# Kernel optimization log

Measured on AMD Instinct MI355X. Metric: run time of the kernel, lower is better.

Reference implementation:

```python
import jax, jax.numpy as jnp
import numpy as np

NH = 12      # attention heads
EPS = 1e-5   # torch nn.LayerNorm default


def _ln(x, g, b):
    m = jnp.mean(x, axis=-1, keepdims=True)
    v = jnp.var(x, axis=-1, keepdims=True)
    return (x - m) * jax.lax.rsqrt(v + EPS) * g + b


def _rel_table(table, n):
    # q_size == k_size == n, table length == 2n-1 -> pure gather, no interpolation
    idx = jnp.arange(n)[:, None] - jnp.arange(n)[None, :] + (n - 1)
    return table[idx]  # (n, n, head_dim)


def _attn2d(x, qkv_w, qkv_b, proj_w, proj_b, rel_h, rel_w):
    B, H, W, C = x.shape
    hd = C // NH
    scale = hd ** -0.5
    N = H * W
    qkv = x.reshape(B, N, C) @ qkv_w + qkv_b                    # (B, N, 3C)
    qkv = qkv.reshape(B, N, 3, NH, hd).transpose(2, 0, 3, 1, 4).reshape(3, B * NH, N, hd)
    q, k, v = qkv[0], qkv[1], qkv[2]
    attn = jnp.einsum('bnd,bmd->bnm', q * scale, k)             # (B*NH, N, N)
    Rh = _rel_table(rel_h, H)
    Rw = _rel_table(rel_w, W)
    rq = q.reshape(B * NH, H, W, hd)                            # unscaled q, as in torch
    bias_h = jnp.einsum('bhwc,hkc->bhwk', rq, Rh)
    bias_w = jnp.einsum('bhwc,wkc->bhwk', rq, Rw)
    attn = (attn.reshape(B * NH, H, W, H, W)
            + bias_h[:, :, :, :, None]
            + bias_w[:, :, :, None, :]).reshape(B * NH, N, N)
    attn = jax.nn.softmax(attn, axis=-1)
    out = (attn @ v).reshape(B, NH, H, W, hd).transpose(0, 2, 3, 1, 4).reshape(B, H, W, C)
    return out @ proj_w + proj_b


def _win_part(x, ws):
    B, H, W, C = x.shape
    ph = (ws - H % ws) % ws
    pw = (ws - W % ws) % ws
    x = jnp.pad(x, ((0, 0), (0, ph), (0, pw), (0, 0)))
    Hp, Wp = H + ph, W + pw
    x = x.reshape(B, Hp // ws, ws, Wp // ws, ws, C).transpose(0, 1, 3, 2, 4, 5)
    return x.reshape(-1, ws, ws, C), (Hp, Wp)


def _win_unpart(wins, ws, pad_hw, hw):
    Hp, Wp = pad_hw
    H, W = hw
    B = wins.shape[0] // (Hp * Wp // ws // ws)
    x = wins.reshape(B, Hp // ws, Wp // ws, ws, ws, -1).transpose(0, 1, 3, 2, 4, 5)
    x = x.reshape(B, Hp, Wp, -1)
    return x[:, :H, :W, :]


def _block(x, ws, ln1g, ln1b, qkvw, qkvb, projw, projb, relh, relw,
           ln2g, ln2b, mw1, mb1, mw2, mb2):
    shortcut = x
    x = _ln(x, ln1g, ln1b)
    if ws > 0:
        H, W = x.shape[1], x.shape[2]
        x, pad_hw = _win_part(x, ws)
    x = _attn2d(x, qkvw, qkvb, projw, projb, relh, relw)
    if ws > 0:
        x = _win_unpart(x, ws, pad_hw, (H, W))
    x = shortcut + x
    h = _ln(x, ln2g, ln2b)
    h = jax.nn.gelu(h @ mw1 + mb1, approximate=False) @ mw2 + mb2
    return x + h


def setup_inputs() -> dict:
    key = jax.random.key(0)
    def rnd(i, shape, s=0.02):
        return jax.random.normal(jax.random.fold_in(key, i), shape, jnp.float32) * s
    C, M, HD = 768, 3072, 64
    d = {
        'x': rnd(0, (1, 3, 1024, 1024), 1.0),
        'patch_w': rnd(1, (16, 16, 3, C)),
        'patch_b': rnd(2, (C,)),
        'pos_embed': rnd(3, (1, 64, 64, C)),
    }
    i = 4
    for s, L in (('1', 27), ('2', 127)):
        for name, shape in (('ln1g', (C,)), ('ln1b', (C,)), ('qkvw', (C, 3 * C)),
                            ('qkvb', (3 * C,)), ('projw', (C, C)), ('projb', (C,)),
                            ('relh', (L, HD)), ('relw', (L, HD)),
                            ('ln2g', (C,)), ('ln2b', (C,)),
                            ('mw1', (C, M)), ('mb1', (M,)), ('mw2', (M, C)), ('mb2', (C,))):
            d[name + s] = rnd(i, shape)
            i += 1
    for s in ('1', '2'):
        d['ln1g' + s] = d['ln1g' + s] + 1.0
        d['ln2g' + s] = d['ln2g' + s] + 1.0
    return d


def reference(x, patch_w, patch_b, pos_embed,
              ln1g1, ln1b1, qkvw1, qkvb1, projw1, projb1, relh1, relw1,
              ln2g1, ln2b1, mw11, mb11, mw21, mb21,
              ln1g2, ln1b2, qkvw2, qkvb2, projw2, projb2, relh2, relw2,
              ln2g2, ln2b2, mw12, mb12, mw22, mb22):
    # patch embed: 16x16 stride-16 conv, output NHWC (B, 64, 64, 768)
    feat = jax.lax.conv_general_dilated(
        x, patch_w, window_strides=(16, 16), padding='VALID',
        dimension_numbers=('NCHW', 'HWIO', 'NHWC'))
    feat = feat + patch_b + pos_embed
    feat = _block(feat, 14, ln1g1, ln1b1, qkvw1, qkvb1, projw1, projb1,
                  relh1, relw1, ln2g1, ln2b1, mw11, mb11, mw21, mb21)
    feat = _block(feat, 0, ln1g2, ln1b2, qkvw2, qkvb2, projw2, projb2,
                  relh2, relw2, ln2g2, ln2b2, mw12, mb12, mw22, mb22)
    return feat
```

## Files before the change

### kernel.cpp

```cpp
#include <hip/hip_runtime.h>


using u16 = unsigned short;
using u32 = unsigned int;
using short8  = __attribute__((ext_vector_type(8))) short;
using floatx4 = __attribute__((ext_vector_type(4))) float;

__device__ __forceinline__ float bfu2f(u16 u) { return __builtin_bit_cast(float, (u32)u << 16); }
__device__ __forceinline__ u16   f2bfu(float f) {
  u32 u = __builtin_bit_cast(u32, f);
  return (u16)((u + 0x7fffu + ((u >> 16) & 1u)) >> 16);
}
__device__ __forceinline__ u32 cvtpk_bf16(float a, float b) {
  u32 r; asm("v_cvt_pk_bf16_f32 %0, %1, %2" : "=v"(r) : "v"(a), "v"(b)); return r;
}
#define DIV14(x) (((x) * 4682) >> 16)
#define WAIT_VM0()   __builtin_amdgcn_s_waitcnt(0x3f70)
#define WAIT_LGKM0() __builtin_amdgcn_s_waitcnt(0xc07f)

__device__ __forceinline__ void gld_lds16(const u16* g, u16* l) {
  __builtin_amdgcn_global_load_lds(
      (const __attribute__((address_space(1))) u32*)g,
      (__attribute__((address_space(3))) u32*)l, 16, 0, 0);
}

__global__ __launch_bounds__(256) void detect_k(const u16* __restrict__ x, int* __restrict__ flag)
{
  __shared__ int tot;
  if (threadIdx.x == 0) tot = 0;
  __syncthreads();
  int cnt = 0;
  for (int i = threadIdx.x; i < 4096; i += 256) {
    int e = (x[2 * i] >> 7) & 0xFF;
    cnt += (e >= 100 && e <= 134) ? 1 : 0;
  }
  atomicAdd(&tot, cnt);
  __syncthreads();
  if (threadIdx.x == 0) *flag = (tot >= 2458) ? 1 : 0;
}

struct CvtEnt { const void* src; int n; int dstoff; };
struct CvtArgs { CvtEnt e[24]; int cnt; };

__global__ __launch_bounds__(256) void tobf_multi_k(CvtArgs a, u16* __restrict__ dst,
                                                    const int* __restrict__ flag)
{
  int gid = blockIdx.x * 256 + threadIdx.x;
  bool isbf = (*flag != 0);
  for (int t = 0; t < a.cnt; ++t)
    if (gid < a.e[t].n)
      dst[a.e[t].dstoff + gid] = isbf ? ((const u16*)a.e[t].src)[gid]
                                      : f2bfu(((const float*)a.e[t].src)[gid]);
}

__global__ __launch_bounds__(256) void tobf4_k(const void* __restrict__ src, u16* __restrict__ dst,
                                               int n4, const int* __restrict__ flag)
{
  int i = blockIdx.x * 256 + threadIdx.x;
  if (i >= n4) return;
  ushort4 o;
  if (*flag) o = ((const ushort4*)src)[i];
  else {
    float4 f = ((const float4*)src)[i];
    o.x = f2bfu(f.x); o.y = f2bfu(f.y); o.z = f2bfu(f.z); o.w = f2bfu(f.w);
  }
  ((ushort4*)dst)[i] = o;
}

__global__ __launch_bounds__(256) void tobfT_k(const void* __restrict__ src, u16* __restrict__ dst,
                                               int K, int N, const int* __restrict__ flag)
{
  __shared__ u16 t[64][65];
  const int n0 = blockIdx.x * 64, k0 = blockIdx.y * 64;
  const int r = threadIdx.x >> 2, c = (threadIdx.x & 3) * 16;
  if (*flag) {
    const u16* s = (const u16*)src + (size_t)(k0 + r) * N + n0 + c;
    union { uint4 v[2]; u16 e[16]; } u;
    u.v[0] = *(const uint4*)s; u.v[1] = *(const uint4*)(s + 8);
    #pragma unroll
    for (int j = 0; j < 16; ++j) t[c + j][r] = u.e[j];
  } else {
    const float* s = (const float*)src + (size_t)(k0 + r) * N + n0 + c;
    #pragma unroll
    for (int j = 0; j < 16; ++j) t[c + j][r] = f2bfu(s[j]);
  }
  __syncthreads();
  union { uint4 v[2]; u16 e[16]; } o;
  #pragma unroll
  for (int j = 0; j < 16; ++j) o.e[j] = t[r][c + j];
  u16* d = dst + (size_t)(n0 + r) * K + k0 + c;
  *(uint4*)d = o.v[0]; *(uint4*)(d + 8) = o.v[1];
}

__global__ __launch_bounds__(256) void im2col_k(const void* __restrict__ xv, u16* __restrict__ a,
                                                const int* __restrict__ flag)
{
  int t = blockIdx.x, tid = threadIdx.x;
  int py = t >> 6, px = t & 63;
  int ky = tid >> 4, kx = tid & 15;
  size_t src = (size_t)(py * 16 + ky) * 1024 + px * 16 + kx;
  u16 v0, v1, v2;
  if (*flag) {
    const u16* x = (const u16*)xv;
    v0 = x[src]; v1 = x[src + 1048576]; v2 = x[src + 2097152];
  } else {
    const float* x = (const float*)xv;
    v0 = f2bfu(x[src]); v1 = f2bfu(x[src + 1048576]); v2 = f2bfu(x[src + 2097152]);
  }
  size_t dst = (size_t)t * 768 + tid * 3;
  a[dst] = v0; a[dst + 1] = v1; a[dst + 2] = v2;
}

__global__ __launch_bounds__(256) void ln_k(const float* __restrict__ x,
                                            const u16* __restrict__ g,
                                            const u16* __restrict__ b,
                                            u16* __restrict__ y)
{
  const int t = blockIdx.x, tid = threadIdx.x;
  const float* xp = x + (size_t)t * 768;
  float v0 = xp[tid], v1 = xp[tid + 256], v2 = xp[tid + 512];
  float s = v0 + v1 + v2;
  float q = v0 * v0 + v1 * v1 + v2 * v2;
  #pragma unroll
  for (int off = 32; off; off >>= 1) { s += __shfl_xor(s, off); q += __shfl_xor(q, off); }
  __shared__ float red[8];
  int wid = tid >> 6, lane = tid & 63;
  if (lane == 0) { red[wid] = s; red[4 + wid] = q; }
  __syncthreads();
  s = red[0] + red[1] + red[2] + red[3];
  q = red[4] + red[5] + red[6] + red[7];
  float mean = s * (1.f / 768.f);
  float var  = q * (1.f / 768.f) - mean * mean;
  float rstd = rsqrtf(var + 1e-5f);
  u16* yp = y + (size_t)t * 768;
  yp[tid]       = f2bfu((v0 - mean) * rstd * bfu2f(g[tid])       + bfu2f(b[tid]));
  yp[tid + 256] = f2bfu((v1 - mean) * rstd * bfu2f(g[tid + 256]) + bfu2f(b[tid + 256]));
  yp[tid + 512] = f2bfu((v2 - mean) * rstd * bfu2f(g[tid + 512]) + bfu2f(b[tid + 512]));
}

__global__ __launch_bounds__(256) void win_part_k(const u16* __restrict__ ln, u16* __restrict__ w)
{
  int vid = blockIdx.x * 256 + threadIdx.x;
  if (vid >= 470400) return;
  size_t idx = (size_t)vid * 8;
  int c = (int)(idx % 768);
  int r = (int)(idx / 768);
  int win = r / 196, tok = r - win * 196;
  int gy = (win / 5) * 14 + tok / 14;
  int gx = (win % 5) * 14 + tok % 14;
  uint4 v = make_uint4(0, 0, 0, 0);
  if (gy < 64 && gx < 64)
    v = *(const uint4*)(ln + ((size_t)(gy * 64 + gx) * 768 + c));
  *(uint4*)(w + idx) = v;
}

enum { MODE_FEAT = 0, MODE_QKV = 1, MODE_RES = 2, MODE_GELU = 3, MODE_OUT = 4 };

template<int BN>
__global__ __launch_bounds__(256) void mgemm_k(
    const u16* __restrict__ A, const u16* __restrict__ Bt, const u16* __restrict__ bias,
    int M, int N, int K, int mode,
    float* __restrict__ outf, u16* __restrict__ outb,
    const float* __restrict__ res, const u16* __restrict__ pos,
    u16* __restrict__ qb, u16* __restrict__ kb, u16* __restrict__ vt, int TW,
    const int* __restrict__ flagp)
{
  constexpr int NWN = BN / 64, NWM = 4 / NWN;
  constexpr int WTM = 128 / NWM;
  constexpr int MS = WTM / 16, NS = 4;
  __shared__ __align__(16) u16 As[2][128 * 32];
  __shared__ __align__(16) u16 Bs[2][BN * 32];
  const int tid = threadIdx.x;
  const int wid = tid >> 6, lane = tid & 63;
  const int l15 = lane & 15, quad = lane >> 4;
  const int wm = wid / NWN, wn = wid % NWN;
  const int m0 = blockIdx.y * 128, n0 = blockIdx.x * BN;

  floatx4 acc[MS][NS];
  #pragma unroll
  for (int i = 0; i < MS; ++i)
    #pragma unroll
    for (int j = 0; j < NS; ++j) acc[i][j] = (floatx4){0.f, 0.f, 0.f, 0.f};

  const int sr = lane >> 2, sc = (lane & 3) * 8;
  const u16* ag0 = A + (size_t)min(m0 + wid * 32 + sr,      M - 1) * K + sc;
  const u16* ag1 = A + (size_t)min(m0 + wid * 32 + 16 + sr, M - 1) * K + sc;
  const u16 *bg0 = nullptr, *bg1 = nullptr;
  if constexpr (BN == 128) {
    bg0 = Bt + (size_t)(n0 + wid * 32 + sr) * K + sc;
    bg1 = Bt + (size_t)(n0 + wid * 32 + 16 + sr) * K + sc;
  } else {
    bg0 = Bt + (size_t)(n0 + wid * 16 + sr) * K + sc;
  }

  auto issue = [&](int buf, int k0) {
    gld_lds16(ag0 + k0, &As[buf][(wid * 32) * 32]);
    gld_lds16(ag1 + k0, &As[buf][(wid * 32 + 16) * 32]);
    if constexpr (BN == 128) {
      gld_lds16(bg0 + k0, &Bs[buf][(wid * 32) * 32]);
      gld_lds16(bg1 + k0, &Bs[buf][(wid * 32 + 16) * 32]);
    } else {
      gld_lds16(bg0 + k0, &Bs[buf][(wid * 16) * 32]);
    }
  };

  issue(0, 0);
  int bufi = 0;
  for (int k0 = 0; k0 < K; k0 += 32, bufi ^= 1) {
    WAIT_VM0();
    __syncthreads();
    if (k0 + 32 < K) issue(bufi ^ 1, k0 + 32);
    short8 af[MS], bf[NS];
    #pragma unroll
    for (int ms = 0; ms < MS; ++ms)
      af[ms] = *(const short8*)&As[bufi][(wm * WTM + ms * 16 + l15) * 32 + quad * 8];
    #pragma unroll
    for (int ns = 0; ns < NS; ++ns)
      bf[ns] = *(const short8*)&Bs[bufi][(wn * 64 + ns * 16 + l15) * 32 + quad * 8];
    #pragma unroll
    for (int ms = 0; ms < MS; ++ms)
      #pragma unroll
      for (int ns = 0; ns < NS; ++ns)
        acc[ms][ns] = __builtin_amdgcn_mfma_f32_16x16x32_bf16(af[ms], bf[ns], acc[ms][ns], 0, 0, 0);
  }

  const bool outbf = (mode == MODE_OUT) ? (*flagp != 0) : false;
  #pragma unroll
  for (int ms = 0; ms < MS; ++ms) {
    const int gmb = m0 + wm * WTM + ms * 16 + quad * 4;
    #pragma unroll
    for (int ns = 0; ns < NS; ++ns) {
      const int gn = n0 + wn * 64 + ns * 16 + l15;
      const float bb = bfu2f(bias[gn]);
      if (mode == MODE_QKV) {
        const int s = gn / 768, nn = gn - s * 768, h = nn >> 6, d = nn & 63;
        #pragma unroll
        for (int r = 0; r < 4; ++r) {
          int gm = gmb + r; if (gm >= M) continue;
          float v = acc[ms][ns][r] + bb;
          int b = gm / TW, tok = gm - b * TW;
          size_t bh = (size_t)(b * 12 + h);
          if (s == 0)      qb[(bh * TW + tok) * 64 + d] = f2bfu(v);
          else if (s == 1) kb[(bh * TW + tok) * 64 + d] = f2bfu(v);
          else             vt[(bh * 64 + d) * TW + tok] = f2bfu(v);
        }
      } else {
        #pragma unroll
        for (int r = 0; r < 4; ++r) {
          int gm = gmb + r; if (gm >= M) continue;
          size_t o = (size_t)gm * N + gn;
          float v = acc[ms][ns][r] + bb;
          if (mode == MODE_FEAT)      outf[o] = v + bfu2f(pos[o]);
          else if (mode == MODE_RES)  outf[o] = v + res[o];
          else if (mode == MODE_GELU) outb[o] = f2bfu(0.5f * v * (1.f + erff(v * 0.70710678f)));
          else {
            float ov = v + res[o];
            if (outbf) outb[o] = f2bfu(ov);
            else       outf[o] = ov;
          }
        }
      }
    }
  }
}

template<int NT, int TD, bool WIN>
__global__ __launch_bounds__(256) void flash_k(
    const u16* __restrict__ qb, const u16* __restrict__ kb, const u16* __restrict__ vt,
    const u16* __restrict__ relh, const u16* __restrict__ relw,
    u16* __restrict__ outb)
{
  constexpr int NTAB = 2 * TD - 1;
  constexpr int KT = (NT + 63) >> 6;
  constexpr float L2E = 1.4426950408889634f;
  constexpr float SC2 = 0.125f * L2E;
  constexpr int RQ  = 0;
  constexpr int RK0 = 4096;
  constexpr int RK1 = WIN ? 4096 : 8192;
  constexpr int RV0 = WIN ? 8192 : 12288;
  constexpr int RV1 = WIN ? 8192 : 16384;
  constexpr int RG  = WIN ? 12288 : 20480;
  constexpr int GWWIN = RG + 64 * 34;
  constexpr int TOT = WIN ? (GWWIN + 64 * 34) : (RG + 64 * 66);
  __shared__ __align__(16) u16 lds[TOT];

  const int tid = threadIdx.x, wid = tid >> 6, lane = tid & 63;
  const int l15 = lane & 15, quad = lane >> 4;
  const int qt = blockIdx.x, bh = blockIdx.y;
  const int q0 = qt * 64;
  const size_t kvbase = (size_t)bh * NT * 64;
  const size_t vbase  = (size_t)bh * 64 * NT;
  const int myrow = wid * 16 + l15;

  auto swb = [](int row, int blk) { return row * 64 + (((blk ^ row) & 7) << 3); };

  {
    const int r = tid >> 2, cb = (tid & 3) * 2;
    const int tok = min(q0 + r, NT - 1);
    const uint4* p = (const uint4*)(qb + kvbase + (size_t)tok * 64 + cb * 8);
    *(uint4*)&lds[RQ + swb(r, cb)]     = p[0];
    *(uint4*)&lds[RQ + swb(r, cb + 1)] = p[1];
  }
  __syncthreads();
  short8 qf[2];
  qf[0] = *(const short8*)&lds[RQ + swb(myrow, quad)];
  qf[1] = *(const short8*)&lds[RQ + swb(myrow, 4 + quad)];
  WAIT_LGKM0();

  auto stageRB = [&](const u16* tab, int rowoff, int maxrow) {
    const int r = tid >> 2, cb = (tid & 3) * 2;
    const int tr = min(rowoff + r, maxrow);
    const uint4* p = (const uint4*)(tab + (size_t)tr * 64 + cb * 8);
    *(uint4*)&lds[RV0 + swb(r, cb)]     = p[0];
    *(uint4*)&lds[RV0 + swb(r, cb + 1)] = p[1];
  };
  auto gpass = [&](int gbase, int gstride, int ncols) {
    for (int ns = 0; ns < ncols / 16; ++ns) {
      floatx4 g = (floatx4){0.f, 0.f, 0.f, 0.f};
      #pragma unroll
      for (int ks = 0; ks < 2; ++ks) {
        short8 b = *(const short8*)&lds[RV0 + swb(ns * 16 + l15, ks * 4 + quad)];
        g = __builtin_amdgcn_mfma_f32_16x16x32_bf16(qf[ks], b, g, 0, 0, 0);
      }
      #pragma unroll
      for (int r = 0; r < 4; ++r)
        lds[gbase + (wid * 16 + quad * 4 + r) * gstride + ns * 16 + l15] = f2bfu(g[r] * L2E);
    }
  };

  float gwv[4][4];
  if constexpr (!WIN) {
    stageRB(relh, qt, NTAB - 1);  __syncthreads();
    gpass(RG, 66, 64);
    __syncthreads();
    stageRB(relw, 0, NTAB - 1);   __syncthreads();
    gpass(RK0, 66, 64);
    #pragma unroll
    for (int kbi = 0; kbi < 4; ++kbi)
      #pragma unroll
      for (int r = 0; r < 4; ++r) {
        const int iw = myrow + 63 - (kbi * 16 + quad * 4 + r);
        if (iw < 64) gwv[kbi][r] = bfu2f(lds[RK0 + myrow * 66 + iw]);
      }
    WAIT_LGKM0();
    __syncthreads();
    stageRB(relw, 64, NTAB - 1);  __syncthreads();
    gpass(RK0, 66, 64);
    #pragma unroll
    for (int kbi = 0; kbi < 4; ++kbi)
      #pragma unroll
      for (int r = 0; r < 4; ++r) {
        const int iw = myrow + 63 - (kbi * 16 + quad * 4 + r);
        if (iw >= 64) gwv[kbi][r] = bfu2f(lds[RK0 + myrow * 66 + iw - 64]);
      }
    WAIT_LGKM0();
  } else {
    stageRB(relh, 0, NTAB - 1);  __syncthreads();
    gpass(RG, 34, 32);
    __syncthreads();
    stageRB(relw, 0, NTAB - 1);  __syncthreads();
    gpass(GWWIN, 34, 32);
  }

  const int srow = lane >> 3;
  const int scol = (((lane & 7) ^ srow) & 7) << 3;
  const u16* kg = kb + kvbase + (size_t)(wid * 16 + srow) * 64 + scol;
  const u16* vg = vt + vbase  + (size_t)(wid * 16 + srow) * NT + scol;
  auto issue = [&](int buf, int kt2) {
    const u16* k0 = kg + (size_t)kt2 * 4096;
    const u16* v0 = vg + kt2 * 64;
    u16* kd = &lds[(buf ? RK1 : RK0) + wid * 16 * 64];
    u16* vd = &lds[(buf ? RV1 : RV0) + wid * 16 * 64];
    gld_lds16(k0,           kd);
    gld_lds16(k0 + 512,     kd + 512);
    gld_lds16(v0,           vd);
    gld_lds16(v0 + 8 * NT,  vd + 512);
  };

  float mI = -3e38f, lI = 0.f;
  floatx4 Oacc[4];
  #pragma unroll
  for (int d = 0; d < 4; ++d) Oacc[d] = (floatx4){0.f, 0.f, 0.f, 0.f};

  int qy = 0, qx = 0;
  if constexpr (WIN) {
    const int tok0 = q0 + myrow;
    qy = DIV14(tok0); qx = tok0 - 14 * qy;
  }

  if constexpr (!WIN) { __syncthreads(); issue(0, 0); }

  for (int kt = 0; kt < KT; ++kt) {
    int RKb, RVb;
    if constexpr (!WIN) {
      WAIT_VM0();
      __syncthreads();
      if (kt + 1 < KT) issue((kt + 1) & 1, kt + 1);
      RKb = (kt & 1) ? RK1 : RK0;
      RVb = (kt & 1) ? RV1 : RV0;
    } else {
      __syncthreads();
      {
        const int r = tid >> 2, cb = (tid & 3) * 2;
        const int key = min(kt * 64 + r, NT - 1);
        const uint4* p = (const uint4*)(kb + kvbase + (size_t)key * 64 + cb * 8);
        *(uint4*)&lds[RK0 + swb(r, cb)]     = p[0];
        *(uint4*)&lds[RK0 + swb(r, cb + 1)] = p[1];
      }
      {
        const int d = tid >> 2, c = (tid & 3) << 4;
        if (kt * 64 + c + 15 < NT) {
          #pragma unroll
          for (int h = 0; h < 4; ++h) {
            uint2 v = *(const uint2*)(vt + vbase + (size_t)d * NT + kt * 64 + c + h * 4);
            const int col = c + h * 4;
            *(uint2*)&lds[RV0 + d * 64 + ((((col >> 3) ^ d) & 7) << 3) + (col & 7)] = v;
          }
        } else {
          #pragma unroll
          for (int j = 0; j < 16; ++j) {
            int key = min(kt * 64 + c + j, NT - 1);
            const int col = c + j;
            lds[RV0 + d * 64 + ((((col >> 3) ^ d) & 7) << 3) + (col & 7)] =
                vt[vbase + (size_t)d * NT + key];
          }
        }
      }
      __syncthreads();
      RKb = RK0; RVb = RV0;
    }

    floatx4 sacc[4];
    #pragma unroll
    for (int kbi = 0; kbi < 4; ++kbi) sacc[kbi] = (floatx4){0.f, 0.f, 0.f, 0.f};
    __builtin_amdgcn_s_setprio(1);
    #pragma unroll
    for (int ks = 0; ks < 2; ++ks)
      #pragma unroll
      for (int kbi = 0; kbi < 4; ++kbi) {
        short8 a = *(const short8*)&lds[RKb + swb(kbi * 16 + l15, ks * 4 + quad)];
        sacc[kbi] = __builtin_amdgcn_mfma_f32_16x16x32_bf16(a, qf[ks], sacc[kbi], 0, 0, 0);
      }
    __builtin_amdgcn_s_setprio(0);

    float sv[4][4];
    if constexpr (!WIN) {
      #pragma unroll
      for (int kbi = 0; kbi < 4; ++kbi)
        #pragma unroll
        for (int r = 0; r < 4; ++r)
          sv[kbi][r] = fmaf(SC2, sacc[kbi][r], gwv[kbi][r]);
    } else {
      #pragma unroll
      for (int kbi = 0; kbi < 4; ++kbi)
        #pragma unroll
        for (int r = 0; r < 4; ++r) {
          const int j = kt * 64 + kbi * 16 + quad * 4 + r;
          const int ky = DIV14(j), kx = j - 14 * ky;
          int ih = qy - ky + 13; ih = max(0, min(ih, 31));
          int iw = qx - kx + 13; iw = max(0, min(iw, 31));
          float s = SC2 * sacc[kbi][r] + bfu2f(lds[RG + myrow * 34 + ih])
                                       + bfu2f(lds[GWWIN + myrow * 34 + iw]);
          sv[kbi][r] = (j < NT) ? s : -1e30f;
        }
    }

    float rm;
    {
      float a0 = fmaxf(fmaxf(sv[0][0], sv[0][1]), fmaxf(sv[0][2], sv[0][3]));
      float a1 = fmaxf(fmaxf(sv[1][0], sv[1][1]), fmaxf(sv[1][2], sv[1][3]));
      float a2 = fmaxf(fmaxf(sv[2][0], sv[2][1]), fmaxf(sv[2][2], sv[2][3]));
      float a3 = fmaxf(fmaxf(sv[3][0], sv[3][1]), fmaxf(sv[3][2], sv[3][3]));
      rm = fmaxf(fmaxf(a0, a1), fmaxf(a2, a3));
    }
    rm = fmaxf(rm, __shfl_xor(rm, 16));
    rm = fmaxf(rm, __shfl_xor(rm, 32));
    float ghv = 0.f;
    if constexpr (!WIN) ghv = bfu2f(lds[RG + myrow * 66 + (63 - kt)]);
    const float mt = rm + ghv;
    const float mn = fmaxf(mI, mt);
    const float t = mn - ghv;

    float rs = 0.f;
    u32 pk[8];
    #pragma unroll
    for (int kbi = 0; kbi < 4; ++kbi) {
      float p0 = __builtin_amdgcn_exp2f(sv[kbi][0] - t);
      float p1 = __builtin_amdgcn_exp2f(sv[kbi][1] - t);
      float p2 = __builtin_amdgcn_exp2f(sv[kbi][2] - t);
      float p3 = __builtin_amdgcn_exp2f(sv[kbi][3] - t);
      rs += (p0 + p1) + (p2 + p3);
      pk[2 * kbi]     = cvtpk_bf16(p0, p1);
      pk[2 * kbi + 1] = cvtpk_bf16(p2, p3);
    }
    rs += __shfl_xor(rs, 16);
    rs += __shfl_xor(rs, 32);

    #pragma unroll
    for (int kbi = 0; kbi < 4; ++kbi) {
      const int col = kbi * 16 + quad * 4;
      uint2 w2; w2.x = pk[2 * kbi]; w2.y = pk[2 * kbi + 1];
      *(uint2*)&lds[RQ + myrow * 64 + ((((col >> 3) ^ myrow) & 7) << 3) + (col & 7)] = w2;
    }

    if (__any(mt > mI)) {
      const float al = __builtin_amdgcn_exp2f(mI - mn);
      mI = mn;
      lI = fmaf(lI, al, rs);
      #pragma unroll
      for (int d = 0; d < 4; ++d) Oacc[d] *= al;
    } else {
      lI += rs;
    }

    __builtin_amdgcn_s_setprio(1);
    #pragma unroll
    for (int ks = 0; ks < 2; ++ks) {
      short8 pb = *(const short8*)&lds[RQ + swb(myrow, ks * 4 + quad)];
      #pragma unroll
      for (int d = 0; d < 4; ++d) {
        short8 a = *(const short8*)&lds[RVb + swb(d * 16 + l15, ks * 4 + quad)];
        Oacc[d] = __builtin_amdgcn_mfma_f32_16x16x32_bf16(a, pb, Oacc[d], 0, 0, 0);
      }
    }
    __builtin_amdgcn_s_setprio(0);
  }

  const float rinv = 1.f / lI;
  const int tok = q0 + myrow;
  u32 ow[8];
  #pragma unroll
  for (int d = 0; d < 4; ++d) {
    ow[2 * d]     = cvtpk_bf16(Oacc[d][0] * rinv, Oacc[d][1] * rinv);
    ow[2 * d + 1] = cvtpk_bf16(Oacc[d][2] * rinv, Oacc[d][3] * rinv);
  }
  if constexpr (WIN) {
    if (tok < NT) {
      const int win = bh / 12, h = bh - win * 12;
      const int ty = DIV14(tok), tx = tok - 14 * ty;
      const int gy = (win / 5) * 14 + ty, gx = (win % 5) * 14 + tx;
      if (gy < 64 && gx < 64) {
        u16* op = outb + (size_t)(gy * 64 + gx) * 768 + h * 64;
        #pragma unroll
        for (int d = 0; d < 4; ++d)
          *(uint2*)(op + d * 16 + quad * 4) = make_uint2(ow[2 * d], ow[2 * d + 1]);
      }
    }
  } else {
    u16* op = outb + (size_t)tok * 768 + bh * 64;
    #pragma unroll
    for (int d = 0; d < 4; ++d)
      *(uint2*)(op + d * 16 + quad * 4) = make_uint2(ow[2 * d], ow[2 * d + 1]);
  }
}

extern "C" void kernel_launch(void* const* d_in, const int* in_sizes, int n_in,
                              void* d_out, int out_size, void* d_ws, size_t ws_size,
                              hipStream_t stream)
{
  const void* x      = d_in[0];
  const void* patchw = d_in[1];
  const void* patchb = d_in[2];
  const void* pos    = d_in[3];
  const void *ln1g1 = d_in[4],  *ln1b1 = d_in[5];
  const void *qkvw1 = d_in[6],  *qkvb1 = d_in[7];
  const void *projw1= d_in[8],  *projb1= d_in[9];
  const void *relh1 = d_in[10], *relw1 = d_in[11];
  const void *ln2g1 = d_in[12], *ln2b1 = d_in[13];
  const void *mw11  = d_in[14], *mb11  = d_in[15];
  const void *mw21  = d_in[16], *mb21  = d_in[17];
  const void *ln1g2 = d_in[18], *ln1b2 = d_in[19];
  const void *qkvw2 = d_in[20], *qkvb2 = d_in[21];
  const void *projw2= d_in[22], *projb2= d_in[23];
  const void *relh2 = d_in[24], *relw2 = d_in[25];
  const void *ln2g2 = d_in[26], *ln2b2 = d_in[27];
  const void *mw12  = d_in[28], *mb12  = d_in[29];
  const void *mw22  = d_in[30], *mb22  = d_in[31];

  char* w = (char*)d_ws;
  int*   FLAG = (int*)w;  w += 64;
  float* R0 = (float*)w;  w += 12582912;
  float* R1 = (float*)w;  w += 12582912;
  u16*   B0 = (u16*)w;    w += 6291456;
  u16*   Wb = (u16*)w;    w += 7526400;
  u16*   QB = (u16*)w;    w += 7526400;
  u16*   KB = (u16*)w;    w += 7526400;
  u16*   VT = (u16*)w;    w += 7526400;
  u16*   Hb = (u16*)w;    w += 25165824;
  u16*   WA = (u16*)w;    w += 14155776;
  u16*   POSb = (u16*)w;  w += 6291456;
  u16*   PRM = (u16*)w;   w += 106560;
  u16*   Ap = Hb;

  constexpr int WA_QKV = 0, WA_PROJ = 1769472, WA_M1 = 2359296, WA_M2 = 4718592;
  constexpr int PRM_PATCHB = 0, PB1 = 768, PBLK = 26240, PB2 = 768 + PBLK;
  constexpr int O_QKVB = 0, O_PROJB = 2304, O_MB1 = 3072, O_MB2 = 6144,
                O_LN1G = 6912, O_LN1B = 7680, O_LN2G = 8448, O_LN2B = 9216,
                O_RELH = 9984, O_RELW = 18112;

  detect_k<<<1, 256, 0, stream>>>((const u16*)x, FLAG);
  CvtArgs ca; int kk = 0;
  auto add = [&](const void* s, int n, int off) { ca.e[kk].src = s; ca.e[kk].n = n; ca.e[kk].dstoff = off; ++kk; };
  add(patchb, 768, PRM_PATCHB);
  add(qkvb1, 2304, PB1 + O_QKVB); add(projb1, 768, PB1 + O_PROJB);
  add(mb11, 3072, PB1 + O_MB1);   add(mb21, 768, PB1 + O_MB2);
  add(ln1g1, 768, PB1 + O_LN1G);  add(ln1b1, 768, PB1 + O_LN1B);
  add(ln2g1, 768, PB1 + O_LN2G);  add(ln2b1, 768, PB1 + O_LN2B);
  add(relh1, 27 * 64, PB1 + O_RELH); add(relw1, 27 * 64, PB1 + O_RELW);
  add(qkvb2, 2304, PB2 + O_QKVB); add(projb2, 768, PB2 + O_PROJB);
  add(mb12, 3072, PB2 + O_MB1);   add(mb22, 768, PB2 + O_MB2);
  add(ln1g2, 768, PB2 + O_LN1G);  add(ln1b2, 768, PB2 + O_LN1B);
  add(ln2g2, 768, PB2 + O_LN2G);  add(ln2b2, 768, PB2 + O_LN2B);
  add(relh2, 127 * 64, PB2 + O_RELH); add(relw2, 127 * 64, PB2 + O_RELW);
  ca.cnt = kk;
  tobf_multi_k<<<32, 256, 0, stream>>>(ca, PRM, FLAG);
  tobf4_k<<<3072, 256, 0, stream>>>(pos, POSb, 786432, FLAG);

  tobfT_k<<<dim3(12, 12), 256, 0, stream>>>(patchw, WA + WA_M1, 768, 768, FLAG);
  im2col_k<<<4096, 256, 0, stream>>>(x, Ap, FLAG);
  mgemm_k<64><<<dim3(12, 32), 256, 0, stream>>>(Ap, WA + WA_M1, PRM + PRM_PATCHB,
      4096, 768, 768, MODE_FEAT, R0, nullptr, nullptr, POSb, nullptr, nullptr, nullptr, 0, FLAG);

  tobfT_k<<<dim3(36, 12), 256, 0, stream>>>(qkvw1, WA + WA_QKV, 768, 2304, FLAG);
  tobfT_k<<<dim3(12, 12), 256, 0, stream>>>(projw1, WA + WA_PROJ, 768, 768, FLAG);
  tobfT_k<<<dim3(48, 12), 256, 0, stream>>>(mw11, WA + WA_M1, 768, 3072, FLAG);
  tobfT_k<<<dim3(12, 48), 256, 0, stream>>>(mw21, WA + WA_M2, 3072, 768, FLAG);

  ln_k<<<4096, 256, 0, stream>>>(R0, PRM + PB1 + O_LN1G, PRM + PB1 + O_LN1B, B0);
  win_part_k<<<1838, 256, 0, stream>>>(B0, Wb);
  mgemm_k<128><<<dim3(18, 39), 256, 0, stream>>>(Wb, WA + WA_QKV, PRM + PB1 + O_QKVB,
      4900, 2304, 768, MODE_QKV, nullptr, nullptr, nullptr, nullptr, QB, KB, VT, 196, FLAG);
  flash_k<196, 14, true><<<dim3(4, 300), 256, 0, stream>>>(QB, KB, VT,
      PRM + PB1 + O_RELH, PRM + PB1 + O_RELW, B0);
  mgemm_k<64><<<dim3(12, 32), 256, 0, stream>>>(B0, WA + WA_PROJ, PRM + PB1 + O_PROJB,
      4096, 768, 768, MODE_RES, R1, nullptr, R0, nullptr, nullptr, nullptr, nullptr, 0, FLAG);
  ln_k<<<4096, 256, 0, stream>>>(R1, PRM + PB1 + O_LN2G, PRM + PB1 + O_LN2B, B0);
  mgemm_k<128><<<dim3(24, 32), 256, 0, stream>>>(B0, WA + WA_M1, PRM + PB1 + O_MB1,
      4096, 3072, 768, MODE_GELU, nullptr, Hb, nullptr, nullptr, nullptr, nullptr, nullptr, 0, FLAG);
  mgemm_k<64><<<dim3(12, 32), 256, 0, stream>>>(Hb, WA + WA_M2, PRM + PB1 + O_MB2,
      4096, 768, 3072, MODE_RES, R0, nullptr, R1, nullptr, nullptr, nullptr, nullptr, 0, FLAG);

  tobfT_k<<<dim3(36, 12), 256, 0, stream>>>(qkvw2, WA + WA_QKV, 768, 2304, FLAG);
  tobfT_k<<<dim3(12, 12), 256, 0, stream>>>(projw2, WA + WA_PROJ, 768, 768, FLAG);
  tobfT_k<<<dim3(48, 12), 256, 0, stream>>>(mw12, WA + WA_M1, 768, 3072, FLAG);
  tobfT_k<<<dim3(12, 48), 256, 0, stream>>>(mw22, WA + WA_M2, 3072, 768, FLAG);

  ln_k<<<4096, 256, 0, stream>>>(R0, PRM + PB2 + O_LN1G, PRM + PB2 + O_LN1B, B0);
  mgemm_k<128><<<dim3(18, 32), 256, 0, stream>>>(B0, WA + WA_QKV, PRM + PB2 + O_QKVB,
      4096, 2304, 768, MODE_QKV, nullptr, nullptr, nullptr, nullptr, QB, KB, VT, 4096, FLAG);
  flash_k<4096, 64, false><<<dim3(64, 12), 256, 0, stream>>>(QB, KB, VT,
      PRM + PB2 + O_RELH, PRM + PB2 + O_RELW, B0);
  mgemm_k<64><<<dim3(12, 32), 256, 0, stream>>>(B0, WA + WA_PROJ, PRM + PB2 + O_PROJB,
      4096, 768, 768, MODE_RES, R1, nullptr, R0, nullptr, nullptr, nullptr, nullptr, 0, FLAG);
  ln_k<<<4096, 256, 0, stream>>>(R1, PRM + PB2 + O_LN2G, PRM + PB2 + O_LN2B, B0);
  mgemm_k<128><<<dim3(24, 32), 256, 0, stream>>>(B0, WA + WA_M1, PRM + PB2 + O_MB1,
      4096, 3072, 768, MODE_GELU, nullptr, Hb, nullptr, nullptr, nullptr, nullptr, nullptr, 0, FLAG);
  mgemm_k<64><<<dim3(12, 32), 256, 0, stream>>>(Hb, WA + WA_M2, PRM + PB2 + O_MB2,
      4096, 768, 3072, MODE_OUT, (float*)d_out, (u16*)d_out, R1, nullptr, nullptr, nullptr, nullptr, 0, FLAG);
}
```

Baseline: 796.6 us.

## Batch weight transposes, fuse LayerNorm with window partition, unroll flash K/V pipeline

Merges the per-weight transpose/convert launches into a single multi-job kernel per block. The patch weight now gets its own workspace slot so it no longer aliases the MLP weight region. Replaces the LayerNorm plus window-partition pair with one kernel that normalizes directly into the padded window layout, removing one intermediate round trip through memory. The global flash-attention loop is unrolled by two with fixed double-buffer pointers and incremental address updates, and the softmax rescale bookkeeping is simplified. The trade-off is more LDS/register pressure from the unrolled body and extra workspace for the weight copies.

```diff
diff --git a/kernel.cpp b/kernel.cpp
--- a/kernel.cpp
+++ b/kernel.cpp
@@ -67,11 +67,24 @@
   ((ushort4*)dst)[i] = o;
 }
 
-__global__ __launch_bounds__(256) void tobfT_k(const void* __restrict__ src, u16* __restrict__ dst,
-                                               int K, int N, const int* __restrict__ flag)
+struct TJob { const void* src; int dstoff; int K; int N; int blk0; };
+struct TArgs { TJob j[6]; int njobs; };
+
+__global__ __launch_bounds__(256) void tobfT_multi_k(TArgs a, u16* __restrict__ wa,
+                                                     const int* __restrict__ flag)
 {
   __shared__ u16 t[64][65];
-  const int n0 = blockIdx.x * 64, k0 = blockIdx.y * 64;
+  const int bid = blockIdx.x;
+  int ji = 0;
+  #pragma unroll
+  for (int q = 1; q < 6; ++q) if (q < a.njobs && bid >= a.j[q].blk0) ji = q;
+  const void* src = a.j[ji].src;
+  u16* dst = wa + a.j[ji].dstoff;
+  const int K = a.j[ji].K, N = a.j[ji].N;
+  const int local = bid - a.j[ji].blk0;
+  const int nx = N >> 6;
+  const int bx = local % nx, by = local / nx;
+  const int n0 = bx * 64, k0 = by * 64;
   const int r = threadIdx.x >> 2, c = (threadIdx.x & 3) * 16;
   if (*flag) {
     const u16* s = (const u16*)src + (size_t)(k0 + r) * N + n0 + c;
@@ -138,20 +151,38 @@
   yp[tid + 512] = f2bfu((v2 - mean) * rstd * bfu2f(g[tid + 512]) + bfu2f(b[tid + 512]));
 }
 
-__global__ __launch_bounds__(256) void win_part_k(const u16* __restrict__ ln, u16* __restrict__ w)
-{
-  int vid = blockIdx.x * 256 + threadIdx.x;
-  if (vid >= 470400) return;
-  size_t idx = (size_t)vid * 8;
-  int c = (int)(idx % 768);
-  int r = (int)(idx / 768);
-  int win = r / 196, tok = r - win * 196;
-  int gy = (win / 5) * 14 + tok / 14;
-  int gx = (win % 5) * 14 + tok % 14;
-  uint4 v = make_uint4(0, 0, 0, 0);
-  if (gy < 64 && gx < 64)
-    v = *(const uint4*)(ln + ((size_t)(gy * 64 + gx) * 768 + c));
-  *(uint4*)(w + idx) = v;
+__global__ __launch_bounds__(256) void ln_win_k(const float* __restrict__ x,
+                                                const u16* __restrict__ g,
+                                                const u16* __restrict__ b,
+                                                u16* __restrict__ wout)
+{
+  const int t = blockIdx.x, tid = threadIdx.x;
+  const int win = t / 196, tok = t - win * 196;
+  const int ty = DIV14(tok), tx = tok - 14 * ty;
+  const int gy = (win / 5) * 14 + ty, gx = (win % 5) * 14 + tx;
+  u16* yp = wout + (size_t)t * 768;
+  if (gy >= 64 || gx >= 64) {
+    yp[tid] = 0; yp[tid + 256] = 0; yp[tid + 512] = 0;
+    return;
+  }
+  const float* xp = x + (size_t)(gy * 64 + gx) * 768;
+  float v0 = xp[tid], v1 = xp[tid + 256], v2 = xp[tid + 512];
+  float s = v0 + v1 + v2;
+  float q = v0 * v0 + v1 * v1 + v2 * v2;
+  #pragma unroll
+  for (int off = 32; off; off >>= 1) { s += __shfl_xor(s, off); q += __shfl_xor(q, off); }
+  __shared__ float red[8];
+  int wid = tid >> 6, lane = tid & 63;
+  if (lane == 0) { red[wid] = s; red[4 + wid] = q; }
+  __syncthreads();
+  s = red[0] + red[1] + red[2] + red[3];
+  q = red[4] + red[5] + red[6] + red[7];
+  float mean = s * (1.f / 768.f);
+  float var  = q * (1.f / 768.f) - mean * mean;
+  float rstd = rsqrtf(var + 1e-5f);
+  yp[tid]       = f2bfu((v0 - mean) * rstd * bfu2f(g[tid])       + bfu2f(b[tid]));
+  yp[tid + 256] = f2bfu((v1 - mean) * rstd * bfu2f(g[tid + 256]) + bfu2f(b[tid + 256]));
+  yp[tid + 512] = f2bfu((v2 - mean) * rstd * bfu2f(g[tid + 512]) + bfu2f(b[tid + 512]));
 }
 
 enum { MODE_FEAT = 0, MODE_QKV = 1, MODE_RES = 2, MODE_GELU = 3, MODE_OUT = 4 };
@@ -364,17 +395,22 @@
 
   const int srow = lane >> 3;
   const int scol = (((lane & 7) ^ srow) & 7) << 3;
-  const u16* kg = kb + kvbase + (size_t)(wid * 16 + srow) * 64 + scol;
-  const u16* vg = vt + vbase  + (size_t)(wid * 16 + srow) * NT + scol;
-  auto issue = [&](int buf, int kt2) {
-    const u16* k0 = kg + (size_t)kt2 * 4096;
-    const u16* v0 = vg + kt2 * 64;
-    u16* kd = &lds[(buf ? RK1 : RK0) + wid * 16 * 64];
-    u16* vd = &lds[(buf ? RV1 : RV0) + wid * 16 * 64];
-    gld_lds16(k0,           kd);
-    gld_lds16(k0 + 512,     kd + 512);
-    gld_lds16(v0,           vd);
-    gld_lds16(v0 + 8 * NT,  vd + 512);
+  const u16* kp  = kb + kvbase + (size_t)(wid * 16 + srow) * 64 + scol;
+  const u16* kp2 = kp + 512;
+  const u16* vp  = vt + vbase  + (size_t)(wid * 16 + srow) * NT + scol;
+  const u16* vp2 = vp + (size_t)8 * NT;
+  u16* const kd0 = &lds[RK0 + wid * 1024];
+  u16* const kd1 = &lds[RK1 + wid * 1024];
+  u16* const vd0 = &lds[RV0 + wid * 1024];
+  u16* const vd1 = &lds[RV1 + wid * 1024];
+  auto issueKV = [&](int buf) {
+    u16* kdb = buf ? kd1 : kd0;
+    u16* vdb = buf ? vd1 : vd0;
+    gld_lds16(kp,  kdb);
+    gld_lds16(kp2, kdb + 512);
+    gld_lds16(vp,  vdb);
+    gld_lds16(vp2, vdb + 512);
+    kp += 4096; kp2 += 4096; vp += 64; vp2 += 64;
   };
 
   float mI = -3e38f, lI = 0.f;
@@ -388,17 +424,117 @@
     qy = DIV14(tok0); qx = tok0 - 14 * qy;
   }
 
-  if constexpr (!WIN) { __syncthreads(); issue(0, 0); }
-
-  for (int kt = 0; kt < KT; ++kt) {
-    int RKb, RVb;
+  auto body = [&](int RKb, int RVb, int kt) {
+    floatx4 sacc[4];
+    #pragma unroll
+    for (int kbi = 0; kbi < 4; ++kbi) sacc[kbi] = (floatx4){0.f, 0.f, 0.f, 0.f};
+    __builtin_amdgcn_s_setprio(1);
+    #pragma unroll
+    for (int ks = 0; ks < 2; ++ks)
+      #pragma unroll
+      for (int kbi = 0; kbi < 4; ++kbi) {
+        short8 a = *(const short8*)&lds[RKb + swb(kbi * 16 + l15, ks * 4 + quad)];
+        sacc[kbi] = __builtin_amdgcn_mfma_f32_16x16x32_bf16(a, qf[ks], sacc[kbi], 0, 0, 0);
+      }
+    __builtin_amdgcn_s_setprio(0);
+
+    float sv[4][4];
     if constexpr (!WIN) {
+      #pragma unroll
+      for (int kbi = 0; kbi < 4; ++kbi)
+        #pragma unroll
+        for (int r = 0; r < 4; ++r)
+          sv[kbi][r] = fmaf(SC2, sacc[kbi][r], gwv[kbi][r]);
+    } else {
+      #pragma unroll
+      for (int kbi = 0; kbi < 4; ++kbi)
+        #pragma unroll
+        for (int r = 0; r < 4; ++r) {
+          const int j = kt * 64 + kbi * 16 + quad * 4 + r;
+          const int ky = DIV14(j), kx = j - 14 * ky;
+          int ih = qy - ky + 13; ih = max(0, min(ih, 31));
+          int iw = qx - kx + 13; iw = max(0, min(iw, 31));
+          float s = SC2 * sacc[kbi][r] + bfu2f(lds[RG + myrow * 34 + ih])
+                                       + bfu2f(lds[GWWIN + myrow * 34 + iw]);
+          sv[kbi][r] = (j < NT) ? s : -1e30f;
+        }
+    }
+
+    float rm;
+    {
+      float a0 = fmaxf(fmaxf(sv[0][0], sv[0][1]), fmaxf(sv[0][2], sv[0][3]));
+      float a1 = fmaxf(fmaxf(sv[1][0], sv[1][1]), fmaxf(sv[1][2], sv[1][3]));
+      float a2 = fmaxf(fmaxf(sv[2][0], sv[2][1]), fmaxf(sv[2][2], sv[2][3]));
+      float a3 = fmaxf(fmaxf(sv[3][0], sv[3][1]), fmaxf(sv[3][2], sv[3][3]));
+      rm = fmaxf(fmaxf(a0, a1), fmaxf(a2, a3));
+    }
+    rm = fmaxf(rm, __shfl_xor(rm, 16));
+    rm = fmaxf(rm, __shfl_xor(rm, 32));
+    float ghv = 0.f;
+    if constexpr (!WIN) ghv = bfu2f(lds[RG + myrow * 66 + (63 - kt)]);
+    const float mt = rm + ghv;
+    const float mn = fmaxf(mI, mt);
+    const float tt = mn - ghv;
+
+    float rs = 0.f;
+    u32 pk[8];
+    #pragma unroll
+    for (int kbi = 0; kbi < 4; ++kbi) {
+      float p0 = __builtin_amdgcn_exp2f(sv[kbi][0] - tt);
+      float p1 = __builtin_amdgcn_exp2f(sv[kbi][1] - tt);
+      float p2 = __builtin_amdgcn_exp2f(sv[kbi][2] - tt);
+      float p3 = __builtin_amdgcn_exp2f(sv[kbi][3] - tt);
+      rs += (p0 + p1) + (p2 + p3);
+      pk[2 * kbi]     = cvtpk_bf16(p0, p1);
+      pk[2 * kbi + 1] = cvtpk_bf16(p2, p3);
+    }
+
+    #pragma unroll
+    for (int kbi = 0; kbi < 4; ++kbi) {
+      const int col = kbi * 16 + quad * 4;
+      uint2 w2; w2.x = pk[2 * kbi]; w2.y = pk[2 * kbi + 1];
+      *(uint2*)&lds[RQ + myrow * 64 + ((((col >> 3) ^ myrow) & 7) << 3) + (col & 7)] = w2;
+    }
+
+    const float al = __builtin_amdgcn_exp2f(mI - mn);
+    if (__any(mt > mI)) {
+      #pragma unroll
+      for (int d = 0; d < 4; ++d) Oacc[d] *= al;
+    }
+    mI = mn;
+
+    __builtin_amdgcn_s_setprio(1);
+    #pragma unroll
+    for (int ks = 0; ks < 2; ++ks) {
+      short8 pb = *(const short8*)&lds[RQ + swb(myrow, ks * 4 + quad)];
+      #pragma unroll
+      for (int d = 0; d < 4; ++d) {
+        short8 a = *(const short8*)&lds[RVb + swb(d * 16 + l15, ks * 4 + quad)];
+        Oacc[d] = __builtin_amdgcn_mfma_f32_16x16x32_bf16(a, pb, Oacc[d], 0, 0, 0);
+      }
+    }
+    __builtin_amdgcn_s_setprio(0);
+
+    rs += __shfl_xor(rs, 16);
+    rs += __shfl_xor(rs, 32);
+    lI = fmaf(lI, al, rs);
+  };
+
+  if constexpr (!WIN) {
+    __syncthreads();
+    issueKV(0);
+    for (int kt = 0; kt < KT; kt += 2) {
       WAIT_VM0();
       __syncthreads();
-      if (kt + 1 < KT) issue((kt + 1) & 1, kt + 1);
-      RKb = (kt & 1) ? RK1 : RK0;
-      RVb = (kt & 1) ? RV1 : RV0;
-    } else {
+      if (kt + 1 < KT) issueKV(1);
+      body(RK0, RV0, kt);
+      WAIT_VM0();
+      __syncthreads();
+      if (kt + 2 < KT) issueKV(0);
+      body(RK1, RV1, kt + 1);
+    }
+  } else {
+    for (int kt = 0; kt < KT; ++kt) {
       __syncthreads();
       {
         const int r = tid >> 2, cb = (tid & 3) * 2;
@@ -427,103 +563,8 @@
         }
       }
       __syncthreads();
-      RKb = RK0; RVb = RV0;
-    }
-
-    floatx4 sacc[4];
-    #pragma unroll
-    for (int kbi = 0; kbi < 4; ++kbi) sacc[kbi] = (floatx4){0.f, 0.f, 0.f, 0.f};
-    __builtin_amdgcn_s_setprio(1);
-    #pragma unroll
-    for (int ks = 0; ks < 2; ++ks)
-      #pragma unroll
-      for (int kbi = 0; kbi < 4; ++kbi) {
-        short8 a = *(const short8*)&lds[RKb + swb(kbi * 16 + l15, ks * 4 + quad)];
-        sacc[kbi] = __builtin_amdgcn_mfma_f32_16x16x32_bf16(a, qf[ks], sacc[kbi], 0, 0, 0);
-      }
-    __builtin_amdgcn_s_setprio(0);
-
-    float sv[4][4];
-    if constexpr (!WIN) {
-      #pragma unroll
-      for (int kbi = 0; kbi < 4; ++kbi)
-        #pragma unroll
-        for (int r = 0; r < 4; ++r)
-          sv[kbi][r] = fmaf(SC2, sacc[kbi][r], gwv[kbi][r]);
-    } else {
-      #pragma unroll
-      for (int kbi = 0; kbi < 4; ++kbi)
-        #pragma unroll
-        for (int r = 0; r < 4; ++r) {
-          const int j = kt * 64 + kbi * 16 + quad * 4 + r;
-          const int ky = DIV14(j), kx = j - 14 * ky;
-          int ih = qy - ky + 13; ih = max(0, min(ih, 31));
-          int iw = qx - kx + 13; iw = max(0, min(iw, 31));
-          float s = SC2 * sacc[kbi][r] + bfu2f(lds[RG + myrow * 34 + ih])
-                                       + bfu2f(lds[GWWIN + myrow * 34 + iw]);
-          sv[kbi][r] = (j < NT) ? s : -1e30f;
-        }
-    }
-
-    float rm;
-    {
-      float a0 = fmaxf(fmaxf(sv[0][0], sv[0][1]), fmaxf(sv[0][2], sv[0][3]));
-      float a1 = fmaxf(fmaxf(sv[1][0], sv[1][1]), fmaxf(sv[1][2], sv[1][3]));
-      float a2 = fmaxf(fmaxf(sv[2][0], sv[2][1]), fmaxf(sv[2][2], sv[2][3]));
-      float a3 = fmaxf(fmaxf(sv[3][0], sv[3][1]), fmaxf(sv[3][2], sv[3][3]));
-      rm = fmaxf(fmaxf(a0, a1), fmaxf(a2, a3));
-    }
-    rm = fmaxf(rm, __shfl_xor(rm, 16));
-    rm = fmaxf(rm, __shfl_xor(rm, 32));
-    float ghv = 0.f;
-    if constexpr (!WIN) ghv = bfu2f(lds[RG + myrow * 66 + (63 - kt)]);
-    const float mt = rm + ghv;
-    const float mn = fmaxf(mI, mt);
-    const float t = mn - ghv;
-
-    float rs = 0.f;
-    u32 pk[8];
-    #pragma unroll
-    for (int kbi = 0; kbi < 4; ++kbi) {
-      float p0 = __builtin_amdgcn_exp2f(sv[kbi][0] - t);
-      float p1 = __builtin_amdgcn_exp2f(sv[kbi][1] - t);
-      float p2 = __builtin_amdgcn_exp2f(sv[kbi][2] - t);
-      float p3 = __builtin_amdgcn_exp2f(sv[kbi][3] - t);
-      rs += (p0 + p1) + (p2 + p3);
-      pk[2 * kbi]     = cvtpk_bf16(p0, p1);
-      pk[2 * kbi + 1] = cvtpk_bf16(p2, p3);
-    }
-    rs += __shfl_xor(rs, 16);
-    rs += __shfl_xor(rs, 32);
-
-    #pragma unroll
-    for (int kbi = 0; kbi < 4; ++kbi) {
-      const int col = kbi * 16 + quad * 4;
-      uint2 w2; w2.x = pk[2 * kbi]; w2.y = pk[2 * kbi + 1];
-      *(uint2*)&lds[RQ + myrow * 64 + ((((col >> 3) ^ myrow) & 7) << 3) + (col & 7)] = w2;
-    }
-
-    if (__any(mt > mI)) {
-      const float al = __builtin_amdgcn_exp2f(mI - mn);
-      mI = mn;
-      lI = fmaf(lI, al, rs);
-      #pragma unroll
-      for (int d = 0; d < 4; ++d) Oacc[d] *= al;
-    } else {
-      lI += rs;
-    }
-
-    __builtin_amdgcn_s_setprio(1);
-    #pragma unroll
-    for (int ks = 0; ks < 2; ++ks) {
-      short8 pb = *(const short8*)&lds[RQ + swb(myrow, ks * 4 + quad)];
-      #pragma unroll
-      for (int d = 0; d < 4; ++d) {
-        short8 a = *(const short8*)&lds[RVb + swb(d * 16 + l15, ks * 4 + quad)];
-        Oacc[d] = __builtin_amdgcn_mfma_f32_16x16x32_bf16(a, pb, Oacc[d], 0, 0, 0);
-      }
-    }
-    __builtin_amdgcn_s_setprio(0);
+      body(RK0, RV0, kt);
+    }
   }
 
   const float rinv = 1.f / lI;
@@ -587,12 +628,13 @@
   u16*   KB = (u16*)w;    w += 7526400;
   u16*   VT = (u16*)w;    w += 7526400;
   u16*   Hb = (u16*)w;    w += 25165824;
-  u16*   WA = (u16*)w;    w += 14155776;
+  u16*   WA = (u16*)w;    w += 15335424;
   u16*   POSb = (u16*)w;  w += 6291456;
   u16*   PRM = (u16*)w;   w += 106560;
   u16*   Ap = Hb;
 
-  constexpr int WA_QKV = 0, WA_PROJ = 1769472, WA_M1 = 2359296, WA_M2 = 4718592;
+  constexpr int WA_QKV = 0, WA_PROJ = 1769472, WA_M1 = 2359296, WA_M2 = 4718592,
+                WA_PATCH = 7077888;
   constexpr int PRM_PATCHB = 0, PB1 = 768, PBLK = 26240, PB2 = 768 + PBLK;
   constexpr int O_QKVB = 0, O_PROJB = 2304, O_MB1 = 3072, O_MB2 = 6144,
                 O_LN1G = 6912, O_LN1B = 7680, O_LN2G = 8448, O_LN2B = 9216,
@@ -616,18 +658,25 @@
   tobf_multi_k<<<32, 256, 0, stream>>>(ca, PRM, FLAG);
   tobf4_k<<<3072, 256, 0, stream>>>(pos, POSb, 786432, FLAG);
 
-  tobfT_k<<<dim3(12, 12), 256, 0, stream>>>(patchw, WA + WA_M1, 768, 768, FLAG);
+  {
+    TArgs ta; int nb = 0, jn = 0;
+    auto addT = [&](const void* s, int dstoff, int K, int N) {
+      ta.j[jn] = { s, dstoff, K, N, nb }; nb += (N >> 6) * (K >> 6); ++jn;
+    };
+    addT(patchw, WA_PATCH, 768, 768);
+    addT(qkvw1,  WA_QKV,   768, 2304);
+    addT(projw1, WA_PROJ,  768, 768);
+    addT(mw11,   WA_M1,    768, 3072);
+    addT(mw21,   WA_M2,   3072, 768);
+    ta.njobs = jn;
+    tobfT_multi_k<<<nb, 256, 0, stream>>>(ta, WA, FLAG);
+  }
+
   im2col_k<<<4096, 256, 0, stream>>>(x, Ap, FLAG);
-  mgemm_k<64><<<dim3(12, 32), 256, 0, stream>>>(Ap, WA + WA_M1, PRM + PRM_PATCHB,
+  mgemm_k<64><<<dim3(12, 32), 256, 0, stream>>>(Ap, WA + WA_PATCH, PRM + PRM_PATCHB,
       4096, 768, 768, MODE_FEAT, R0, nullptr, nullptr, POSb, nullptr, nullptr, nullptr, 0, FLAG);
 
-  tobfT_k<<<dim3(36, 12), 256, 0, stream>>>(qkvw1, WA + WA_QKV, 768, 2304, FLAG);
-  tobfT_k<<<dim3(12, 12), 256, 0, stream>>>(projw1, WA + WA_PROJ, 768, 768, FLAG);
-  tobfT_k<<<dim3(48, 12), 256, 0, stream>>>(mw11, WA + WA_M1, 768, 3072, FLAG);
-  tobfT_k<<<dim3(12, 48), 256, 0, stream>>>(mw21, WA + WA_M2, 3072, 768, FLAG);
-
-  ln_k<<<4096, 256, 0, stream>>>(R0, PRM + PB1 + O_LN1G, PRM + PB1 + O_LN1B, B0);
-  win_part_k<<<1838, 256, 0, stream>>>(B0, Wb);
+  ln_win_k<<<4900, 256, 0, stream>>>(R0, PRM + PB1 + O_LN1G, PRM + PB1 + O_LN1B, Wb);
   mgemm_k<128><<<dim3(18, 39), 256, 0, stream>>>(Wb, WA + WA_QKV, PRM + PB1 + O_QKVB,
       4900, 2304, 768, MODE_QKV, nullptr, nullptr, nullptr, nullptr, QB, KB, VT, 196, FLAG);
   flash_k<196, 14, true><<<dim3(4, 300), 256, 0, stream>>>(QB, KB, VT,
@@ -640,10 +689,18 @@
   mgemm_k<64><<<dim3(12, 32), 256, 0, stream>>>(Hb, WA + WA_M2, PRM + PB1 + O_MB2,
       4096, 768, 3072, MODE_RES, R0, nullptr, R1, nullptr, nullptr, nullptr, nullptr, 0, FLAG);
 
-  tobfT_k<<<dim3(36, 12), 256, 0, stream>>>(qkvw2, WA + WA_QKV, 768, 2304, FLAG);
-  tobfT_k<<<dim3(12, 12), 256, 0, stream>>>(projw2, WA + WA_PROJ, 768, 768, FLAG);
-  tobfT_k<<<dim3(48, 12), 256, 0, stream>>>(mw12, WA + WA_M1, 768, 3072, FLAG);
-  tobfT_k<<<dim3(12, 48), 256, 0, stream>>>(mw22, WA + WA_M2, 3072, 768, FLAG);
+  {
+    TArgs ta; int nb = 0, jn = 0;
+    auto addT = [&](const void* s, int dstoff, int K, int N) {
+      ta.j[jn] = { s, dstoff, K, N, nb }; nb += (N >> 6) * (K >> 6); ++jn;
+    };
+    addT(qkvw2,  WA_QKV,  768, 2304);
+    addT(projw2, WA_PROJ, 768, 768);
+    addT(mw12,   WA_M1,   768, 3072);
+    addT(mw22,   WA_M2,  3072, 768);
+    ta.njobs = jn;
+    tobfT_multi_k<<<nb, 256, 0, stream>>>(ta, WA, FLAG);
+  }
 
   ln_k<<<4096, 256, 0, stream>>>(R0, PRM + PB2 + O_LN1G, PRM + PB2 + O_LN1B, B0);
   mgemm_k<128><<<dim3(18, 32), 256, 0, stream>>>(B0, WA + WA_QKV, PRM + PB2 + O_QKVB,
```

Result: faster. 778.6 us (-2.3%).
